# Kernel optimization log

Measured on AMD Instinct MI355X. Metric: run time of the kernel, lower is better.

Reference implementation:

```python
import jax, jax.numpy as jnp
import numpy as np

N = 4096
IN_F = 256
H = 8
F = 64  # out_features per head
ALPHA = 0.2
NEG_BIG = -9e15


def setup_inputs() -> dict:
    key = jax.random.key(0)
    k1, k2, k3, k4 = jax.random.split(key, 4)
    h = jax.random.normal(k1, (N, IN_F), dtype=jnp.float32)
    adj = jax.random.randint(k2, (N, N), 0, 2, dtype=jnp.int32)
    W = jax.random.normal(k3, (IN_F, H * F), dtype=jnp.float32) * (1.0 / np.sqrt(IN_F))
    a = jax.random.normal(k4, (H, 2 * F), dtype=jnp.float32) * (1.0 / np.sqrt(2 * F))
    bias = jnp.zeros((H * F,), dtype=jnp.float32)
    return {"h": h, "adj": adj, "W": W, "a": a, "bias": bias}


def reference(h, adj, W, a, bias):
    n = h.shape[0]
    Wh = (h @ W).reshape(n, H, F)               # [N,H,F]
    a1 = a[:, :F]                                # [H,F]
    a2 = a[:, F:]                                # [H,F]
    attn_1 = jnp.einsum('nhf,hf->nh', Wh, a1)    # [N,H]
    attn_2 = jnp.einsum('nhf,hf->nh', Wh, a2)    # [N,H]
    e = jax.nn.leaky_relu(attn_1[:, None, :] + attn_2[None, :, :], negative_slope=ALPHA)  # [N,N,H]
    e = jnp.where(adj[..., None] > 0, e, NEG_BIG)
    attn = jax.nn.softmax(e, axis=1)             # softmax over source nodes j
    h_prime = jnp.einsum('ijh,jhf->ihf', attn, Wh)  # [N,H,F]
    return h_prime.reshape(n, H * F) + bias
```

## Files before the change

### kernel.cpp

```cpp
#include <hip/hip_runtime.h>
#include <hip/hip_bf16.h>

typedef __bf16 bf16;
typedef __attribute__((ext_vector_type(4)))  __bf16 bf16x4;
typedef __attribute__((ext_vector_type(8)))  __bf16 bf16x8;
typedef __attribute__((ext_vector_type(4)))  float  f32x4;
typedef __attribute__((ext_vector_type(16))) float  f32x16;
typedef __attribute__((ext_vector_type(4)))  unsigned u32x4;

#define NN   4096
#define INF  256
#define HH   8
#define FF   64
#define HF   512
#define ALPHA_ 0.2f
#define NW   128


__global__ __launch_bounds__(256) void k_pack(const int* __restrict__ adj,
                                              unsigned* __restrict__ bits)
{
    const int t   = blockIdx.x * 256 + threadIdx.x;
    const int row = t >> 7;
    const int jw  = t & 127;
    const int* p  = adj + (size_t)row * NN + (jw << 5);
    unsigned m = 0u;
#pragma unroll
    for (int k = 0; k < 8; ++k) {
        const int4 v = *(const int4*)(p + (k << 2));
        m |= (v.x != 0 ? 1u : 0u) << (4 * k);
        m |= (v.y != 0 ? 1u : 0u) << (4 * k + 1);
        m |= (v.z != 0 ? 1u : 0u) << (4 * k + 2);
        m |= (v.w != 0 ? 1u : 0u) << (4 * k + 3);
    }
    bits[t] = m;
}

__global__ __launch_bounds__(256) void k_wht(const float* __restrict__ A,
                                             const float* __restrict__ W,
                                             bf16* __restrict__ WhTt)
{
    __shared__ bf16 Bs[64][36];
    const int bid = blockIdx.x;
    const int mt = (bid >> 3) << 6;
    const int nt = (bid & 7) << 6;
    const int tid = threadIdx.x;
    const int wv  = tid >> 6;
    const int l   = tid & 63;
    const int l15 = l & 15;
    const int lq  = l >> 4;

    f32x4 acc[4];
#pragma unroll
    for (int nb = 0; nb < 4; ++nb) acc[nb] = (f32x4)0.0f;

    const int krow = tid >> 3;
    const int ncol = (tid & 7) << 3;

    for (int kb = 0; kb < INF; kb += 32) {
        const float4 w0 = *(const float4*)&W[(kb + krow) * HF + nt + ncol];
        const float4 w1 = *(const float4*)&W[(kb + krow) * HF + nt + ncol + 4];
        __syncthreads();
        Bs[ncol + 0][krow] = (bf16)w0.x; Bs[ncol + 1][krow] = (bf16)w0.y;
        Bs[ncol + 2][krow] = (bf16)w0.z; Bs[ncol + 3][krow] = (bf16)w0.w;
        Bs[ncol + 4][krow] = (bf16)w1.x; Bs[ncol + 5][krow] = (bf16)w1.y;
        Bs[ncol + 6][krow] = (bf16)w1.z; Bs[ncol + 7][krow] = (bf16)w1.w;
        __syncthreads();

        const float* pA = A + (mt + wv * 16 + l15) * INF + kb + (lq << 2);
        const float4 a0 = *(const float4*)pA;
        const float4 a1 = *(const float4*)(pA + 16);
        bf16x8 af;
        af[0] = (bf16)a0.x; af[1] = (bf16)a0.y; af[2] = (bf16)a0.z; af[3] = (bf16)a0.w;
        af[4] = (bf16)a1.x; af[5] = (bf16)a1.y; af[6] = (bf16)a1.z; af[7] = (bf16)a1.w;

#pragma unroll
        for (int nb = 0; nb < 4; ++nb) {
            const bf16* pB = &Bs[(nb << 4) + l15][lq << 2];
            bf16x4 blo = *(const bf16x4*)pB;
            bf16x4 bhi = *(const bf16x4*)(pB + 16);
            bf16x8 bf = __builtin_shufflevector(blo, bhi, 0,1,2,3,4,5,6,7);
            acc[nb] = __builtin_amdgcn_mfma_f32_16x16x32_bf16(af, bf, acc[nb], 0, 0, 0);
        }
    }

    const int m0 = mt + wv * 16 + (lq << 2);
#pragma unroll
    for (int nb = 0; nb < 4; ++nb) {
        const int col = nt + (nb << 4) + l15;
        bf16x4 o;
#pragma unroll
        for (int r = 0; r < 4; ++r) o[r] = (bf16)acc[nb][r];
        const int hd_ = col >> 6, row_ = col & 63;
        bf16* dst = WhTt + (((size_t)(hd_ << 8) + (m0 >> 4)) << 10)
                  + (row_ << 4) + (m0 & 15);
        *(bf16x4*)dst = o;
    }
}

__global__ __launch_bounds__(256) void k_scores(const bf16* __restrict__ WhTt,
                                                const float* __restrict__ a,
                                                float* __restrict__ E1, float* __restrict__ F1,
                                                bf16* __restrict__ E2b, bf16* __restrict__ F2b)
{
    const int h = blockIdx.x >> 4;
    const int i = ((blockIdx.x & 15) << 8) + threadIdx.x;
    const bf16* wb = WhTt + (((size_t)(h << 8) + (i >> 4)) << 10) + (i & 15);
    float t1 = 0.f, t2 = 0.f;
#pragma unroll 16
    for (int f = 0; f < FF; ++f) {
        float w = (float)wb[f << 4];
        t1 += w * a[h * 128 + f];
        t2 += w * a[h * 128 + 64 + f];
    }
    E1[h * NN + i]  = __expf(t1);
    F1[h * NN + i]  = __expf(ALPHA_ * t1);
    E2b[h * NN + i] = (bf16)__expf(t2);
    F2b[h * NN + i] = (bf16)__expf(ALPHA_ * t2);
}

#define DECL_STAGE(P) \
    unsigned P##_bw; \
    bf16x8 P##_ea, P##_fa, P##_b0, P##_b1;

#define LOAD_STAGE(P, s) do { \
    const int jb_ = jwb + ((s) << 4); \
    const bf16* tb_ = whb + ((s) << 10); \
    P##_bw = (unsigned)bitrow16[(s)]; \
    P##_ea = *(const bf16x8*)(e2r + jb_); \
    P##_fa = *(const bf16x8*)(f2r + jb_); \
    P##_b0 = *(const bf16x8*)(tb_ + (l31 << 4) + (lh << 3)); \
    P##_b1 = *(const bf16x8*)(tb_ + ((32 + l31) << 4) + (lh << 3)); \
} while (0)

#define COMPUTE_STAGE(P) do { \
    const unsigned bsel_ = (P##_bw >> sh0) & 0xffu; \
    bf16x8 pa_; \
    _Pragma("unroll") \
    for (int k_ = 0; k_ < 8; ++k_) { \
        const float w_ = fmaxf(e1 * (float)P##_ea[k_], f1 * (float)P##_fa[k_]); \
        pa_[k_] = (bf16)w_; \
    } \
    u32x4 pm_ = __builtin_bit_cast(u32x4, pa_); \
    _Pragma("unroll") \
    for (int d_ = 0; d_ < 4; ++d_) pm_[d_] &= lut4[(bsel_ >> (2 * d_)) & 3u]; \
    pa_ = __builtin_bit_cast(bf16x8, pm_); \
    acc0 = __builtin_amdgcn_mfma_f32_32x32x16_bf16(pa_, P##_b0, acc0, 0, 0, 0); \
    acc1 = __builtin_amdgcn_mfma_f32_32x32x16_bf16(pa_, P##_b1, acc1, 0, 0, 0); \
    accd = __builtin_amdgcn_mfma_f32_32x32x16_bf16(pa_, ones, accd, 0, 0, 0); \
} while (0)

__global__ __launch_bounds__(512, 3) void k_gat(const unsigned* __restrict__ bits,
                                                const bf16* __restrict__ WhTt,
                                                const float* __restrict__ E1, const float* __restrict__ F1,
                                                const bf16* __restrict__ E2b, const bf16* __restrict__ F2b,
                                                const float* __restrict__ bias,
                                                float* __restrict__ out)
{
    __shared__ float red2[2][32][64];
    __shared__ float dred[8][32];
    __shared__ unsigned lut4[4];

    const int bid = blockIdx.x;
    const int hd = bid & 7;
    const int ib = bid >> 3;

    const int tid = threadIdx.x;
    const int wv  = tid >> 6;
    const int l   = tid & 63;
    const int l31 = l & 31;
    const int lh  = l >> 5;

    if (tid < 4) lut4[tid] = (tid & 1 ? 0x0000FFFFu : 0u) | (tid & 2 ? 0xFFFF0000u : 0u);
    __syncthreads();

    const int i = (ib << 5) + l31;

    const float e1 = E1[hd * NN + i];
    const float f1 = F1[hd * NN + i];

    f32x16 acc0 = (f32x16)0.f, acc1 = (f32x16)0.f, accd = (f32x16)0.f;

    bf16x8 ones;
#pragma unroll
    for (int k = 0; k < 8; ++k) ones[k] = (bf16)1.0f;

    const unsigned short* bitrow16 =
        (const unsigned short*)(bits + (size_t)i * NW) + (wv << 5);
    const bf16* e2r = E2b + hd * NN;
    const bf16* f2r = F2b + hd * NN;
    const bf16* whb = WhTt + ((size_t)hd << 18) + ((size_t)(wv << 5) << 10);

    const int jwb = (wv << 9) + (lh << 3);
    const int sh0 = lh << 3;

    DECL_STAGE(A); DECL_STAGE(B);

    LOAD_STAGE(A, 0);
#pragma unroll 1
    for (int t = 0; t < 15; ++t) {
        LOAD_STAGE(B, 2 * t + 1); COMPUTE_STAGE(A);
        LOAD_STAGE(A, 2 * t + 2); COMPUTE_STAGE(B);
    }
    LOAD_STAGE(B, 31); COMPUTE_STAGE(A); COMPUTE_STAGE(B);

    if (l31 == 0) {
#pragma unroll
        for (int r = 0; r < 16; ++r) {
            dred[wv][(r & 3) + 8 * (r >> 2) + 4 * lh] = accd[r];
        }
    }

    if (wv < 2) {
        float* rb = &red2[wv][0][0];
#pragma unroll
        for (int g = 0; g < 4; ++g) {
            const int ir = (g << 3) + (lh << 2);
#pragma unroll
            for (int r = 0; r < 4; ++r) {
                rb[(ir + r) * 64 + l31     ] = acc0[4*g + r];
                rb[(ir + r) * 64 + 32 + l31] = acc1[4*g + r];
            }
        }
    }
    __syncthreads();
    if (wv == 2 || wv == 3) {
        float* rb = &red2[wv - 2][0][0];
#pragma unroll
        for (int g = 0; g < 4; ++g) {
            const int ir = (g << 3) + (lh << 2);
#pragma unroll
            for (int r = 0; r < 4; ++r) {
                rb[(ir + r) * 64 + l31     ] += acc0[4*g + r];
                rb[(ir + r) * 64 + 32 + l31] += acc1[4*g + r];
            }
        }
    }
    __syncthreads();
    if (wv == 4 || wv == 5) {
        float* rb = &red2[wv - 4][0][0];
#pragma unroll
        for (int g = 0; g < 4; ++g) {
            const int ir = (g << 3) + (lh << 2);
#pragma unroll
            for (int r = 0; r < 4; ++r) {
                rb[(ir + r) * 64 + l31     ] += acc0[4*g + r];
                rb[(ir + r) * 64 + 32 + l31] += acc1[4*g + r];
            }
        }
    }
    __syncthreads();
    if (wv == 6 || wv == 7) {
        float* rb = &red2[wv - 6][0][0];
#pragma unroll
        for (int g = 0; g < 4; ++g) {
            const int ir = (g << 3) + (lh << 2);
#pragma unroll
            for (int r = 0; r < 4; ++r) {
                rb[(ir + r) * 64 + l31     ] += acc0[4*g + r];
                rb[(ir + r) * 64 + 32 + l31] += acc1[4*g + r];
            }
        }
    }
    __syncthreads();

    const int iloc = tid >> 4;
    const int c0   = (tid & 15) << 2;
    const float dsum = dred[0][iloc] + dred[1][iloc] + dred[2][iloc] + dred[3][iloc]
                     + dred[4][iloc] + dred[5][iloc] + dred[6][iloc] + dred[7][iloc];
    const float rd = 1.0f / dsum;
    f32x4 o;
#pragma unroll
    for (int r = 0; r < 4; ++r) {
        const float sv = red2[0][iloc][c0 + r] + red2[1][iloc][c0 + r];
        o[r] = sv * rd + bias[(hd << 6) + c0 + r];
    }
    *(f32x4*)&out[(size_t)((ib << 5) + iloc) * HF + (hd << 6) + c0] = o;
}

extern "C" void kernel_launch(void* const* d_in, const int* in_sizes, int n_in,
                              void* d_out, int out_size, void* d_ws, size_t ws_size,
                              hipStream_t stream) {
    const float* h    = (const float*)d_in[0];
    const int*   adj  = (const int*)d_in[1];
    const float* W    = (const float*)d_in[2];
    const float* a    = (const float*)d_in[3];
    const float* bias = (const float*)d_in[4];
    float* out = (float*)d_out;

    char* ws = (char*)d_ws;
    bf16*     WhTt = (bf16*)ws;
    float*    E1   = (float*)(ws + (size_t)(4 << 20));
    float*    F1   = E1 + HH * NN;
    bf16*     E2b  = (bf16*)(F1 + HH * NN);
    bf16*     F2b  = E2b + HH * NN;
    unsigned* bits = (unsigned*)(ws + (size_t)(4 << 20) + (384 << 10));

    hipLaunchKernelGGL(k_pack,   dim3(2048), dim3(256), 0, stream, adj, bits);
    hipLaunchKernelGGL(k_wht,    dim3(512),  dim3(256), 0, stream, h, W, WhTt);
    hipLaunchKernelGGL(k_scores, dim3(128),  dim3(256), 0, stream, WhTt, a, E1, F1, E2b, F2b);
    hipLaunchKernelGGL(k_gat,    dim3(1024), dim3(512), 0, stream, bits, WhTt, E1, F1, E2b, F2b, bias, out);
}
```

Baseline: 83.85 us.

## Factor row score out of softmax weights, sum denominator on VALU, triple-buffer loads

The per-row factor exp(t1) is pulled out of the attention weight: the weight becomes max(exp(t2), exp(-0.8*t1)*exp(0.2*t2)), since that factor cancels in the softmax normalisation. This replaces two per-row scalars with one and removes one multiply per element. The softmax denominator is now a per-lane scalar sum plus one cross-lane shuffle, which drops the third MFMA against a ones vector. Adjacency masking is a per-element select instead of a LUT bitmask in shared memory. The load/compute pipeline goes from two stages to three to hide more latency, at the cost of extra registers under the 512-thread, 3-block launch bounds.

New measurement: 79.21 us (median of 2 runs). 5.5% less time.

```diff
diff --git a/kernel.cpp b/kernel.cpp
--- a/kernel.cpp
+++ b/kernel.cpp
@@ -6,7 +6,6 @@
 typedef __attribute__((ext_vector_type(8)))  __bf16 bf16x8;
 typedef __attribute__((ext_vector_type(4)))  float  f32x4;
 typedef __attribute__((ext_vector_type(16))) float  f32x16;
-typedef __attribute__((ext_vector_type(4)))  unsigned u32x4;
 
 #define NN   4096
 #define INF  256
@@ -100,7 +99,7 @@
 
 __global__ __launch_bounds__(256) void k_scores(const bf16* __restrict__ WhTt,
                                                 const float* __restrict__ a,
-                                                float* __restrict__ E1, float* __restrict__ F1,
+                                                float* __restrict__ cF,
                                                 bf16* __restrict__ E2b, bf16* __restrict__ F2b)
 {
     const int h = blockIdx.x >> 4;
@@ -113,8 +112,7 @@
         t1 += w * a[h * 128 + f];
         t2 += w * a[h * 128 + 64 + f];
     }
-    E1[h * NN + i]  = __expf(t1);
-    F1[h * NN + i]  = __expf(ALPHA_ * t1);
+    cF[h * NN + i]  = __expf(-0.8f * t1);
     E2b[h * NN + i] = (bf16)__expf(t2);
     F2b[h * NN + i] = (bf16)__expf(ALPHA_ * t2);
 }
@@ -138,28 +136,23 @@
     bf16x8 pa_; \
     _Pragma("unroll") \
     for (int k_ = 0; k_ < 8; ++k_) { \
-        const float w_ = fmaxf(e1 * (float)P##_ea[k_], f1 * (float)P##_fa[k_]); \
-        pa_[k_] = (bf16)w_; \
+        float w_ = ((bsel_ >> k_) & 1u) \
+                 ? fmaxf((float)P##_ea[k_], c * (float)P##_fa[k_]) : 0.f; \
+        den += w_; pa_[k_] = (bf16)w_; \
     } \
-    u32x4 pm_ = __builtin_bit_cast(u32x4, pa_); \
-    _Pragma("unroll") \
-    for (int d_ = 0; d_ < 4; ++d_) pm_[d_] &= lut4[(bsel_ >> (2 * d_)) & 3u]; \
-    pa_ = __builtin_bit_cast(bf16x8, pm_); \
     acc0 = __builtin_amdgcn_mfma_f32_32x32x16_bf16(pa_, P##_b0, acc0, 0, 0, 0); \
     acc1 = __builtin_amdgcn_mfma_f32_32x32x16_bf16(pa_, P##_b1, acc1, 0, 0, 0); \
-    accd = __builtin_amdgcn_mfma_f32_32x32x16_bf16(pa_, ones, accd, 0, 0, 0); \
 } while (0)
 
 __global__ __launch_bounds__(512, 3) void k_gat(const unsigned* __restrict__ bits,
                                                 const bf16* __restrict__ WhTt,
-                                                const float* __restrict__ E1, const float* __restrict__ F1,
+                                                const float* __restrict__ cF,
                                                 const bf16* __restrict__ E2b, const bf16* __restrict__ F2b,
                                                 const float* __restrict__ bias,
                                                 float* __restrict__ out)
 {
     __shared__ float red2[2][32][64];
     __shared__ float dred[8][32];
-    __shared__ unsigned lut4[4];
 
     const int bid = blockIdx.x;
     const int hd = bid & 7;
@@ -171,19 +164,12 @@
     const int l31 = l & 31;
     const int lh  = l >> 5;
 
-    if (tid < 4) lut4[tid] = (tid & 1 ? 0x0000FFFFu : 0u) | (tid & 2 ? 0xFFFF0000u : 0u);
-    __syncthreads();
-
     const int i = (ib << 5) + l31;
 
-    const float e1 = E1[hd * NN + i];
-    const float f1 = F1[hd * NN + i];
-
-    f32x16 acc0 = (f32x16)0.f, acc1 = (f32x16)0.f, accd = (f32x16)0.f;
-
-    bf16x8 ones;
-#pragma unroll
-    for (int k = 0; k < 8; ++k) ones[k] = (bf16)1.0f;
+    const float c = cF[hd * NN + i];
+
+    f32x16 acc0 = (f32x16)0.f, acc1 = (f32x16)0.f;
+    float den = 0.f;
 
     const unsigned short* bitrow16 =
         (const unsigned short*)(bits + (size_t)i * NW) + (wv << 5);
@@ -194,22 +180,19 @@
     const int jwb = (wv << 9) + (lh << 3);
     const int sh0 = lh << 3;
 
-    DECL_STAGE(A); DECL_STAGE(B);
-
-    LOAD_STAGE(A, 0);
+    DECL_STAGE(A); DECL_STAGE(B); DECL_STAGE(C);
+
+    LOAD_STAGE(A, 0); LOAD_STAGE(B, 1);
 #pragma unroll 1
-    for (int t = 0; t < 15; ++t) {
-        LOAD_STAGE(B, 2 * t + 1); COMPUTE_STAGE(A);
-        LOAD_STAGE(A, 2 * t + 2); COMPUTE_STAGE(B);
-    }
-    LOAD_STAGE(B, 31); COMPUTE_STAGE(A); COMPUTE_STAGE(B);
-
-    if (l31 == 0) {
-#pragma unroll
-        for (int r = 0; r < 16; ++r) {
-            dred[wv][(r & 3) + 8 * (r >> 2) + 4 * lh] = accd[r];
-        }
-    }
+    for (int t = 0; t < 10; ++t) {
+        LOAD_STAGE(C, 3 * t + 2); COMPUTE_STAGE(A);
+        LOAD_STAGE(A, 3 * t + 3); COMPUTE_STAGE(B);
+        LOAD_STAGE(B, 3 * t + 4); COMPUTE_STAGE(C);
+    }
+    COMPUTE_STAGE(A); COMPUTE_STAGE(B);
+
+    den += __shfl_xor(den, 32, 64);
+    if (l < 32) dred[wv][l31] = den;
 
     if (wv < 2) {
         float* rb = &red2[wv][0][0];
@@ -290,14 +273,13 @@
 
     char* ws = (char*)d_ws;
     bf16*     WhTt = (bf16*)ws;
-    float*    E1   = (float*)(ws + (size_t)(4 << 20));
-    float*    F1   = E1 + HH * NN;
-    bf16*     E2b  = (bf16*)(F1 + HH * NN);
+    float*    cF   = (float*)(ws + (size_t)(4 << 20));
+    bf16*     E2b  = (bf16*)(cF + HH * NN);
     bf16*     F2b  = E2b + HH * NN;
     unsigned* bits = (unsigned*)(ws + (size_t)(4 << 20) + (384 << 10));
 
     hipLaunchKernelGGL(k_pack,   dim3(2048), dim3(256), 0, stream, adj, bits);
     hipLaunchKernelGGL(k_wht,    dim3(512),  dim3(256), 0, stream, h, W, WhTt);
-    hipLaunchKernelGGL(k_scores, dim3(128),  dim3(256), 0, stream, WhTt, a, E1, F1, E2b, F2b);
-    hipLaunchKernelGGL(k_gat,    dim3(1024), dim3(512), 0, stream, bits, WhTt, E1, F1, E2b, F2b, bias, out);
-}
+    hipLaunchKernelGGL(k_scores, dim3(128),  dim3(256), 0, stream, WhTt, a, cF, E2b, F2b);
+    hipLaunchKernelGGL(k_gat,    dim3(1024), dim3(512), 0, stream, bits, WhTt, cF, E2b, F2b, bias, out);
+}
```
